# Performance work log

Measured on AMD Instinct MI355X. Metric: run time of the kernel, lower is better.

The kernel has to match this reference:

```python
import jax, jax.numpy as jnp
import numpy as np

D_HIDN = 64
SCALE = 1.0 / np.sqrt(D_HIDN).astype(np.float32)
MASK_FILL = -1e9


def setup_inputs() -> dict:
    key = jax.random.key(0)
    kq, kk, kv, km = jax.random.split(key, 4)
    B, H, S, D = 4, 16, 2048, 64
    Q = jax.random.normal(kq, (B, H, S, D), dtype=jnp.float32)
    K = jax.random.normal(kk, (B, H, S, D), dtype=jnp.float32)
    V = jax.random.normal(kv, (B, H, S, D), dtype=jnp.float32)
    attn_mask = jax.random.randint(km, (B, H, S, S), 0, 2).astype(jnp.bool_)
    return {"Q": Q, "K": K, "V": V, "attn_mask": attn_mask}


def reference(Q, K, V, attn_mask):
    # scores = Q K^T * scale  -> [B,H,S,S]
    scores = jnp.einsum("bhqd,bhkd->bhqk", Q, K) * SCALE
    scores = jnp.where(attn_mask, MASK_FILL, scores)
    attn_prob = jax.nn.softmax(scores, axis=-1)
    # dropout is identity in eval / deterministic reference
    context = jnp.einsum("bhqk,bhkd->bhqd", attn_prob, V)
    return (context, attn_prob)
```

## Files before the change

### kernel.cpp

```cpp
#include <hip/hip_runtime.h>
#include <stdint.h>

#define SEQ 2048
#define DIM 64
#define QBLK 16
#define NWAVE 8
#define KPW 256
#define NCT 16
#define NCHUNK 8
#define THREADS 512
#define SCALE 0.125f
#define LOG2E 1.4426950408889634f
#define PSTR 40
#define VPAD 18
#define NTSTR (32*VPAD + 8)

typedef __attribute__((ext_vector_type(4))) float f32x4;
typedef __attribute__((ext_vector_type(4))) int   i32x4;
typedef __attribute__((ext_vector_type(8))) __bf16 bf16x8;

static __device__ __forceinline__ unsigned bfbits(float x) {
    union { __bf16 b; unsigned short u; } cv; cv.b = (__bf16)x; return (unsigned)cv.u;
}
static __device__ __forceinline__ float lo16(unsigned u) { return __uint_as_float(u << 16); }
static __device__ __forceinline__ float hi16(unsigned u) { return __uint_as_float(u & 0xffff0000u); }
static __device__ __forceinline__ bf16x8 cvt8(f32x4 a, f32x4 b) {
    bf16x8 f;
    f[0]=(__bf16)a[0]; f[1]=(__bf16)a[1]; f[2]=(__bf16)a[2]; f[3]=(__bf16)a[3];
    f[4]=(__bf16)b[0]; f[5]=(__bf16)b[1]; f[6]=(__bf16)b[2]; f[7]=(__bf16)b[3];
    return f;
}

struct WaveBuf {
    union {
        __bf16 vbuf[4 * NTSTR];
        float  ctx[QBLK * DIM];
    };
};
struct SharedT {
    WaveBuf sw[NWAVE];
    __bf16 plds[NWAVE][QBLK][PSTR];
    float red_m[QBLK][NWAVE];
    float red_s[QBLK][NWAVE];
};

__global__ __launch_bounds__(THREADS, 4)
void sdpa_mfma11(const float* __restrict__ Q, const float* __restrict__ K,
                 const float* __restrict__ V, const int* __restrict__ mask,
                 float* __restrict__ ctx_out, float* __restrict__ prob_out) {
    __shared__ SharedT su;

    const int rb   = ((blockIdx.x & 7) << 10) + (blockIdx.x >> 3);
    const int bh   = rb >> 7;
    const int q0   = (rb & 127) * QBLK;
    const int t    = threadIdx.x;
    const int lane = t & 63;
    const int w    = t >> 6;
    const int g    = lane >> 4;
    const int c    = lane & 15;

    const size_t bh_off = (size_t)bh * SEQ * DIM;
    const float* Qb = Q + bh_off;
    const float* Kb = K + bh_off;
    const float* Vb = V + bh_off;
    const int*   Mb = mask + (size_t)bh * SEQ * SEQ;
    const int wbase = w * KPW;

    bf16x8 qf[2];
    {
        const float* qr = Qb + (size_t)(q0 + c) * DIM + 8 * g;
        qf[0] = cvt8(*(const f32x4*)(qr),      *(const f32x4*)(qr + 4));
        qf[1] = cvt8(*(const f32x4*)(qr + 32), *(const f32x4*)(qr + 36));
    }

    unsigned sc_pk[2 * NCT];
    f32x4 kr[4];
    i32x4 mraw[2];
    {
        const float* k0 = Kb + (size_t)(wbase + c) * DIM + 8 * g;
        kr[0] = *(const f32x4*)(k0);      kr[1] = *(const f32x4*)(k0 + 4);
        kr[2] = *(const f32x4*)(k0 + 32); kr[3] = *(const f32x4*)(k0 + 36);
        mraw[0] = *(const i32x4*)(Mb + (size_t)(q0 + c) * SEQ + wbase + 4 * g);
    }
    #pragma unroll
    for (int ct = 0; ct < NCT; ++ct) {
        if (ct + 1 < NCT)
            mraw[(ct + 1) & 1] = *(const i32x4*)(Mb + (size_t)(q0 + c) * SEQ + wbase + (ct + 1) * 16 + 4 * g);
        bf16x8 kf0 = cvt8(kr[0], kr[1]);
        bf16x8 kf1 = cvt8(kr[2], kr[3]);
        if (ct + 1 < NCT) {
            const float* kn = Kb + (size_t)(wbase + (ct + 1) * 16 + c) * DIM + 8 * g;
            kr[0] = *(const f32x4*)(kn);      kr[1] = *(const f32x4*)(kn + 4);
            kr[2] = *(const f32x4*)(kn + 32); kr[3] = *(const f32x4*)(kn + 36);
        }
        f32x4 acc = {0.f, 0.f, 0.f, 0.f};
        acc = __builtin_amdgcn_mfma_f32_16x16x32_bf16(kf0, qf[0], acc, 0, 0, 0);
        acc = __builtin_amdgcn_mfma_f32_16x16x32_bf16(kf1, qf[1], acc, 0, 0, 0);
        i32x4 mm = mraw[ct & 1];
        float x0 = mm[0] ? -1e9f : acc[0] * SCALE;
        float x1 = mm[1] ? -1e9f : acc[1] * SCALE;
        float x2 = mm[2] ? -1e9f : acc[2] * SCALE;
        float x3 = mm[3] ? -1e9f : acc[3] * SCALE;
        sc_pk[2 * ct]     = bfbits(x0) | (bfbits(x1) << 16);
        sc_pk[2 * ct + 1] = bfbits(x2) | (bfbits(x3) << 16);
    }

    float mx = -3e38f;
    #pragma unroll
    for (int i = 0; i < 2 * NCT; ++i)
        mx = fmaxf(mx, fmaxf(lo16(sc_pk[i]), hi16(sc_pk[i])));
    mx = fmaxf(mx, __shfl_xor(mx, 16));
    mx = fmaxf(mx, __shfl_xor(mx, 32));
    if (g == 0) su.red_m[c][w] = mx;
    __syncthreads();
    float M = su.red_m[c][0];
    #pragma unroll
    for (int i = 1; i < NWAVE; ++i) M = fmaxf(M, su.red_m[c][i]);

    float sum = 0.f;
    #pragma unroll
    for (int i = 0; i < 2 * NCT; ++i) {
        float e0 = exp2f((lo16(sc_pk[i]) - M) * LOG2E);
        float e1 = exp2f((hi16(sc_pk[i]) - M) * LOG2E);
        sum += e0 + e1;
        sc_pk[i] = bfbits(e0) | (bfbits(e1) << 16);
    }
    sum += __shfl_xor(sum, 16);
    sum += __shfl_xor(sum, 32);
    if (g == 0) su.red_s[c][w] = sum;
    __syncthreads();
    float S = 0.f;
    #pragma unroll
    for (int i = 0; i < NWAVE; ++i) S += su.red_s[c][i];
    const float inv = 1.0f / S;
    float invr[4];
    #pragma unroll
    for (int jr = 0; jr < 4; ++jr) invr[jr] = __shfl(inv, 4 * g + jr);

    f32x4 cacc[4];
    #pragma unroll
    for (int nt = 0; nt < 4; ++nt) cacc[nt] = (f32x4){0.f, 0.f, 0.f, 0.f};

    const int r_st = lane >> 4;
    const int cw   = (4 * c) & 15;
    const int ntw  = c >> 2;
    float* prow = prob_out + ((size_t)bh * SEQ + (q0 + c)) * SEQ + wbase;
    __bf16* vbufW = su.sw[w].vbuf;

    #pragma unroll
    for (int cc = 0; cc < NCHUNK; ++cc) {
        const float* vsrc = Vb + (size_t)(wbase + cc * 32 + r_st) * DIM + 4 * c;
        f32x4 vraw[4];
        #pragma unroll
        for (int i = 0; i < 4; ++i)
            vraw[i] = *(const f32x4*)(vsrc + (size_t)(4 * i) * DIM);
        #pragma unroll
        for (int i = 0; i < 4; ++i) {
            ushort2 lo_, hi_;
            lo_.x = (unsigned short)bfbits(vraw[i][0]);
            lo_.y = (unsigned short)bfbits(vraw[i][1]);
            hi_.x = (unsigned short)bfbits(vraw[i][2]);
            hi_.y = (unsigned short)bfbits(vraw[i][3]);
            __bf16* p = &vbufW[ntw * NTSTR + (4 * i + r_st) * VPAD + cw];
            *(ushort2*)p = lo_;
            *(ushort2*)(p + 2) = hi_;
        }
        #pragma unroll
        for (int i = 0; i < 4; ++i)
            vraw[i] = *(const f32x4*)(vsrc + (size_t)(16 + 4 * i) * DIM);
        #pragma unroll
        for (int i = 0; i < 4; ++i) {
            ushort2 lo_, hi_;
            lo_.x = (unsigned short)bfbits(vraw[i][0]);
            lo_.y = (unsigned short)bfbits(vraw[i][1]);
            hi_.x = (unsigned short)bfbits(vraw[i][2]);
            hi_.y = (unsigned short)bfbits(vraw[i][3]);
            __bf16* p = &vbufW[ntw * NTSTR + (16 + 4 * i + r_st) * VPAD + cw];
            *(ushort2*)p = lo_;
            *(ushort2*)(p + 2) = hi_;
        }

        unsigned pkA0 = sc_pk[4 * cc],     pkA1 = sc_pk[4 * cc + 1];
        unsigned pkB0 = sc_pk[4 * cc + 2], pkB1 = sc_pk[4 * cc + 3];
        {
            f32x4 pnA = { lo16(pkA0) * inv, hi16(pkA0) * inv, lo16(pkA1) * inv, hi16(pkA1) * inv };
            f32x4 pnB = { lo16(pkB0) * inv, hi16(pkB0) * inv, lo16(pkB1) * inv, hi16(pkB1) * inv };
            *(f32x4*)(prow + 32 * cc + 4 * g)      = pnA;
            *(f32x4*)(prow + 32 * cc + 16 + 4 * g) = pnB;
        }
        {
            uint2 ua; ua.x = pkA0; ua.y = pkA1;
            uint2 ub; ub.x = pkB0; ub.y = pkB1;
            *(uint2*)&su.plds[w][c][4 * g]      = ua;
            *(uint2*)&su.plds[w][c][16 + 4 * g] = ub;
        }
        bf16x8 pf = *(const bf16x8*)&su.plds[w][c][8 * g];

        bf16x8 vfr[4];
        #pragma unroll
        for (int nt = 0; nt < 4; ++nt) {
            bf16x8 f;
            #pragma unroll
            for (int j = 0; j < 8; ++j)
                f[j] = vbufW[nt * NTSTR + (8 * g + j) * VPAD + c];
            vfr[nt] = f;
        }

        __builtin_amdgcn_s_setprio(1);
        #pragma unroll
        for (int nt = 0; nt < 4; ++nt)
            cacc[nt] = __builtin_amdgcn_mfma_f32_16x16x32_bf16(pf, vfr[nt], cacc[nt], 0, 0, 0);
        __builtin_amdgcn_s_setprio(0);
    }

    #pragma unroll
    for (int nt = 0; nt < 4; ++nt)
        #pragma unroll
        for (int jr = 0; jr < 4; ++jr)
            su.sw[w].ctx[(4 * g + jr) * DIM + nt * 16 + c] = cacc[nt][jr] * invr[jr];
    __syncthreads();
    {
        int e = t * 2;
        float2 a = make_float2(0.f, 0.f);
        #pragma unroll
        for (int i = 0; i < NWAVE; ++i) {
            float2 v = *(const float2*)&su.sw[i].ctx[e];
            a.x += v.x; a.y += v.y;
        }
        *(float2*)(ctx_out + ((size_t)bh * SEQ + q0) * DIM + e) = a;
    }
}

extern "C" void kernel_launch(void* const* d_in, const int* in_sizes, int n_in,
                              void* d_out, int out_size, void* d_ws, size_t ws_size,
                              hipStream_t stream) {
    const float* Q = (const float*)d_in[0];
    const float* K = (const float*)d_in[1];
    const float* V = (const float*)d_in[2];
    const int* mask = (const int*)d_in[3];
    float* ctx  = (float*)d_out;
    float* prob = (float*)d_out + (size_t)4 * 16 * SEQ * DIM;

    dim3 grid(64 * (SEQ / QBLK));
    dim3 block(THREADS);
    sdpa_mfma11<<<grid, block, 0, stream>>>(Q, K, V, mask, ctx, prob);
}
```

Baseline: 1.032 ms.

## Batch mask loads into bitmasks and prefetch V chunks one step ahead

Mask loads become deep batches of four 16-int vectors that are compressed into 32-bit bitmasks. This raises memory-level parallelism on the mask stream, which is the largest input. Masking moves to a separate pass over the packed bf16 scores after the QK MFMA loop. V for the first chunk is loaded before the softmax reductions, and each later chunk is prefetched during the current one to hide global latency. The cost is more live registers (mask quads and V prefetch buffers), which could lower occupancy or cause spills.

```diff
diff --git a/kernel.cpp b/kernel.cpp
--- a/kernel.cpp
+++ b/kernel.cpp
@@ -30,6 +30,9 @@
     f[4]=(__bf16)b[0]; f[5]=(__bf16)b[1]; f[6]=(__bf16)b[2]; f[7]=(__bf16)b[3];
     return f;
 }
+static __device__ __forceinline__ unsigned nib4(i32x4 mm) {
+    return (mm[0]?1u:0u) | (mm[1]?2u:0u) | (mm[2]?4u:0u) | (mm[3]?8u:0u);
+}
 
 struct WaveBuf {
     union {
@@ -45,7 +48,7 @@
 };
 
 __global__ __launch_bounds__(THREADS, 4)
-void sdpa_mfma11(const float* __restrict__ Q, const float* __restrict__ K,
+void sdpa_mfma12(const float* __restrict__ Q, const float* __restrict__ K,
                  const float* __restrict__ V, const int* __restrict__ mask,
                  float* __restrict__ ctx_out, float* __restrict__ prob_out) {
     __shared__ SharedT su;
@@ -74,18 +77,40 @@
     }
 
     unsigned sc_pk[2 * NCT];
+    unsigned mbits0 = 0u, mbits1 = 0u;
+    const int* mrow = Mb + (size_t)(q0 + c) * SEQ + wbase + 4 * g;
+    i32x4 mq0[4], mq1[4];
+    #pragma unroll
+    for (int j = 0; j < 4; ++j) mq0[j] = *(const i32x4*)(mrow + 16 * j);
+    #pragma unroll
+    for (int j = 0; j < 4; ++j) mq1[j] = *(const i32x4*)(mrow + 16 * (4 + j));
+
     f32x4 kr[4];
-    i32x4 mraw[2];
     {
         const float* k0 = Kb + (size_t)(wbase + c) * DIM + 8 * g;
         kr[0] = *(const f32x4*)(k0);      kr[1] = *(const f32x4*)(k0 + 4);
         kr[2] = *(const f32x4*)(k0 + 32); kr[3] = *(const f32x4*)(k0 + 36);
-        mraw[0] = *(const i32x4*)(Mb + (size_t)(q0 + c) * SEQ + wbase + 4 * g);
-    }
+    }
+
     #pragma unroll
     for (int ct = 0; ct < NCT; ++ct) {
-        if (ct + 1 < NCT)
-            mraw[(ct + 1) & 1] = *(const i32x4*)(Mb + (size_t)(q0 + c) * SEQ + wbase + (ct + 1) * 16 + 4 * g);
+        if (ct == 4) {
+            #pragma unroll
+            for (int j = 0; j < 4; ++j) mbits0 |= nib4(mq0[j]) << (4 * j);
+            #pragma unroll
+            for (int j = 0; j < 4; ++j) mq0[j] = *(const i32x4*)(mrow + 16 * (8 + j));
+        }
+        if (ct == 8) {
+            #pragma unroll
+            for (int j = 0; j < 4; ++j) mbits0 |= nib4(mq1[j]) << (4 * (4 + j));
+            #pragma unroll
+            for (int j = 0; j < 4; ++j) mq1[j] = *(const i32x4*)(mrow + 16 * (12 + j));
+        }
+        if (ct == 12) {
+            #pragma unroll
+            for (int j = 0; j < 4; ++j) mbits1 |= nib4(mq0[j]) << (4 * j);
+        }
+
         bf16x8 kf0 = cvt8(kr[0], kr[1]);
         bf16x8 kf1 = cvt8(kr[2], kr[3]);
         if (ct + 1 < NCT) {
@@ -96,11 +121,33 @@
         f32x4 acc = {0.f, 0.f, 0.f, 0.f};
         acc = __builtin_amdgcn_mfma_f32_16x16x32_bf16(kf0, qf[0], acc, 0, 0, 0);
         acc = __builtin_amdgcn_mfma_f32_16x16x32_bf16(kf1, qf[1], acc, 0, 0, 0);
-        i32x4 mm = mraw[ct & 1];
-        float x0 = mm[0] ? -1e9f : acc[0] * SCALE;
-        float x1 = mm[1] ? -1e9f : acc[1] * SCALE;
-        float x2 = mm[2] ? -1e9f : acc[2] * SCALE;
-        float x3 = mm[3] ? -1e9f : acc[3] * SCALE;
+        sc_pk[2 * ct]     = bfbits(acc[0] * SCALE) | (bfbits(acc[1] * SCALE) << 16);
+        sc_pk[2 * ct + 1] = bfbits(acc[2] * SCALE) | (bfbits(acc[3] * SCALE) << 16);
+    }
+
+    const int r_st = lane >> 4;
+    const int cw   = (4 * c) & 15;
+    const int ntw  = c >> 2;
+    f32x4 vrawA[4], vrawB[4];
+    {
+        const float* vsrc = Vb + (size_t)(wbase + r_st) * DIM + 4 * c;
+        #pragma unroll
+        for (int i = 0; i < 4; ++i) {
+            vrawA[i] = *(const f32x4*)(vsrc + (size_t)(4 * i) * DIM);
+            vrawB[i] = *(const f32x4*)(vsrc + (size_t)(16 + 4 * i) * DIM);
+        }
+    }
+
+    #pragma unroll
+    for (int j = 0; j < 4; ++j) mbits1 |= nib4(mq1[j]) << (4 * (4 + j));
+
+    #pragma unroll
+    for (int ct = 0; ct < NCT; ++ct) {
+        unsigned nib = ((ct < 8) ? (mbits0 >> (4 * ct)) : (mbits1 >> (4 * (ct - 8)))) & 0xFu;
+        float x0 = (nib & 1u) ? -1e9f : lo16(sc_pk[2 * ct]);
+        float x1 = (nib & 2u) ? -1e9f : hi16(sc_pk[2 * ct]);
+        float x2 = (nib & 4u) ? -1e9f : lo16(sc_pk[2 * ct + 1]);
+        float x3 = (nib & 8u) ? -1e9f : hi16(sc_pk[2 * ct + 1]);
         sc_pk[2 * ct]     = bfbits(x0) | (bfbits(x1) << 16);
         sc_pk[2 * ct + 1] = bfbits(x2) | (bfbits(x3) << 16);
     }
@@ -141,43 +188,40 @@
     #pragma unroll
     for (int nt = 0; nt < 4; ++nt) cacc[nt] = (f32x4){0.f, 0.f, 0.f, 0.f};
 
-    const int r_st = lane >> 4;
-    const int cw   = (4 * c) & 15;
-    const int ntw  = c >> 2;
     float* prow = prob_out + ((size_t)bh * SEQ + (q0 + c)) * SEQ + wbase;
     __bf16* vbufW = su.sw[w].vbuf;
 
     #pragma unroll
     for (int cc = 0; cc < NCHUNK; ++cc) {
-        const float* vsrc = Vb + (size_t)(wbase + cc * 32 + r_st) * DIM + 4 * c;
-        f32x4 vraw[4];
-        #pragma unroll
-        for (int i = 0; i < 4; ++i)
-            vraw[i] = *(const f32x4*)(vsrc + (size_t)(4 * i) * DIM);
         #pragma unroll
         for (int i = 0; i < 4; ++i) {
             ushort2 lo_, hi_;
-            lo_.x = (unsigned short)bfbits(vraw[i][0]);
-            lo_.y = (unsigned short)bfbits(vraw[i][1]);
-            hi_.x = (unsigned short)bfbits(vraw[i][2]);
-            hi_.y = (unsigned short)bfbits(vraw[i][3]);
+            lo_.x = (unsigned short)bfbits(vrawA[i][0]);
+            lo_.y = (unsigned short)bfbits(vrawA[i][1]);
+            hi_.x = (unsigned short)bfbits(vrawA[i][2]);
+            hi_.y = (unsigned short)bfbits(vrawA[i][3]);
             __bf16* p = &vbufW[ntw * NTSTR + (4 * i + r_st) * VPAD + cw];
             *(ushort2*)p = lo_;
             *(ushort2*)(p + 2) = hi_;
         }
         #pragma unroll
-        for (int i = 0; i < 4; ++i)
-            vraw[i] = *(const f32x4*)(vsrc + (size_t)(16 + 4 * i) * DIM);
-        #pragma unroll
         for (int i = 0; i < 4; ++i) {
             ushort2 lo_, hi_;
-            lo_.x = (unsigned short)bfbits(vraw[i][0]);
-            lo_.y = (unsigned short)bfbits(vraw[i][1]);
-            hi_.x = (unsigned short)bfbits(vraw[i][2]);
-            hi_.y = (unsigned short)bfbits(vraw[i][3]);
+            lo_.x = (unsigned short)bfbits(vrawB[i][0]);
+            lo_.y = (unsigned short)bfbits(vrawB[i][1]);
+            hi_.x = (unsigned short)bfbits(vrawB[i][2]);
+            hi_.y = (unsigned short)bfbits(vrawB[i][3]);
             __bf16* p = &vbufW[ntw * NTSTR + (16 + 4 * i + r_st) * VPAD + cw];
             *(ushort2*)p = lo_;
             *(ushort2*)(p + 2) = hi_;
+        }
+        if (cc + 1 < NCHUNK) {
+            const float* vsrc = Vb + (size_t)(wbase + (cc + 1) * 32 + r_st) * DIM + 4 * c;
+            #pragma unroll
+            for (int i = 0; i < 4; ++i) {
+                vrawA[i] = *(const f32x4*)(vsrc + (size_t)(4 * i) * DIM);
+                vrawB[i] = *(const f32x4*)(vsrc + (size_t)(16 + 4 * i) * DIM);
+            }
         }
 
         unsigned pkA0 = sc_pk[4 * cc],     pkA1 = sc_pk[4 * cc + 1];
@@ -243,5 +287,5 @@
 
     dim3 grid(64 * (SEQ / QBLK));
     dim3 block(THREADS);
-    sdpa_mfma11<<<grid, block, 0, stream>>>(Q, K, V, mask, ctx, prob);
-}
+    sdpa_mfma12<<<grid, block, 0, stream>>>(Q, K, V, mask, ctx, prob);
+}
```

Result: faster. 1.010 ms (-2.1%).

## Process two 16-row query blocks per workgroup with wave-local softmax stats

Applied to the files above, without the earlier changes.

Each workgroup now handles 32 query rows as two 16-row halves, so the bf16 V tiles staged in LDS feed MFMAs for both halves. This halves the V reloads and conversions per query row and halves the grid. Softmax max and sum are computed per wave and merged across waves with exp rescaling, which drops one block barrier. The mask is batch-loaded and packed into bit nibbles to overlap its global reads with the QK^T MFMAs, and the V loads are software-pipelined. In exchange, register pressure rises from holding two score arrays, and occupancy may drop under the launch bound of four blocks.

```diff
diff --git a/kernel.cpp b/kernel.cpp
--- a/kernel.cpp
+++ b/kernel.cpp
@@ -6,7 +6,6 @@
 #define QBLK 16
 #define NWAVE 8
 #define KPW 256
-#define NCT 16
 #define NCHUNK 8
 #define THREADS 512
 #define SCALE 0.125f
@@ -29,6 +28,9 @@
     f[0]=(__bf16)a[0]; f[1]=(__bf16)a[1]; f[2]=(__bf16)a[2]; f[3]=(__bf16)a[3];
     f[4]=(__bf16)b[0]; f[5]=(__bf16)b[1]; f[6]=(__bf16)b[2]; f[7]=(__bf16)b[3];
     return f;
+}
+static __device__ __forceinline__ unsigned nib4(i32x4 mm) {
+    return (mm[0]?1u:0u) | (mm[1]?2u:0u) | (mm[2]?4u:0u) | (mm[3]?8u:0u);
 }
 
 struct WaveBuf {
@@ -39,20 +41,82 @@
 };
 struct SharedT {
     WaveBuf sw[NWAVE];
-    __bf16 plds[NWAVE][QBLK][PSTR];
-    float red_m[QBLK][NWAVE];
-    float red_s[QBLK][NWAVE];
+    __bf16 pldsA[NWAVE][QBLK][PSTR];
+    __bf16 pldsB[NWAVE][QBLK][PSTR];
+    float red_m[2][QBLK][NWAVE];
+    float red_s[2][QBLK][NWAVE];
 };
 
+#define QKT_HALF(MROWP, QFP, SCP, MBITSV, TB, LASTH)                           \
+  {                                                                            \
+    i32x4 mq0_ = *(const i32x4*)((MROWP) + 16*((TB)+0));                       \
+    i32x4 mq1_ = *(const i32x4*)((MROWP) + 16*((TB)+1));                       \
+    i32x4 mq2_ = *(const i32x4*)((MROWP) + 16*((TB)+2));                       \
+    i32x4 mq3_ = *(const i32x4*)((MROWP) + 16*((TB)+3));                       \
+    i32x4 mq4_ = *(const i32x4*)((MROWP) + 16*((TB)+4));                       \
+    i32x4 mq5_ = *(const i32x4*)((MROWP) + 16*((TB)+5));                       \
+    i32x4 mq6_ = *(const i32x4*)((MROWP) + 16*((TB)+6));                       \
+    i32x4 mq7_ = *(const i32x4*)((MROWP) + 16*((TB)+7));                       \
+    __builtin_amdgcn_sched_barrier(0);                                         \
+    _Pragma("unroll")                                                          \
+    for (int ct_ = 0; ct_ < 8; ++ct_) {                                        \
+      if (ct_ == 3)                                                            \
+        MBITSV |= nib4(mq0_) | (nib4(mq1_) << 4) | (nib4(mq2_) << 8)           \
+                  | (nib4(mq3_) << 12);                                        \
+      bf16x8 kf0_ = cvt8(kr[0], kr[1]);                                        \
+      bf16x8 kf1_ = cvt8(kr[2], kr[3]);                                        \
+      if (!(LASTH) || ct_ < 7) {                                               \
+        const int nti_ = ((TB) + ct_ + 1) & 15;                                \
+        const float* kn_ = Kb + (size_t)(wbase + nti_ * 16 + c) * DIM + 8 * g; \
+        kr[0] = *(const f32x4*)(kn_);      kr[1] = *(const f32x4*)(kn_ + 4);   \
+        kr[2] = *(const f32x4*)(kn_ + 32); kr[3] = *(const f32x4*)(kn_ + 36);  \
+      }                                                                        \
+      f32x4 acc_ = {0.f, 0.f, 0.f, 0.f};                                       \
+      acc_ = __builtin_amdgcn_mfma_f32_16x16x32_bf16(kf0_, (QFP)[0], acc_, 0, 0, 0); \
+      acc_ = __builtin_amdgcn_mfma_f32_16x16x32_bf16(kf1_, (QFP)[1], acc_, 0, 0, 0); \
+      (SCP)[2*((TB)+ct_)]   = bfbits(acc_[0]*SCALE) | (bfbits(acc_[1]*SCALE) << 16); \
+      (SCP)[2*((TB)+ct_)+1] = bfbits(acc_[2]*SCALE) | (bfbits(acc_[3]*SCALE) << 16); \
+    }                                                                          \
+    MBITSV |= (nib4(mq4_) << 16) | (nib4(mq5_) << 20) | (nib4(mq6_) << 24)     \
+              | (nib4(mq7_) << 28);                                            \
+  }
+
+#define SMAX_SWEEP(SCP, MB0, MB1, MXV, SSV)                                    \
+  float MXV = -3e38f;                                                          \
+  _Pragma("unroll")                                                            \
+  for (int ct_ = 0; ct_ < 16; ++ct_) {                                         \
+    unsigned nib_ = ((ct_ < 8) ? ((MB0) >> (4*ct_)) : ((MB1) >> (4*(ct_-8)))) & 0xFu; \
+    float x0_ = (nib_ & 1u) ? -1e9f : lo16((SCP)[2*ct_]);                      \
+    float x1_ = (nib_ & 2u) ? -1e9f : hi16((SCP)[2*ct_]);                      \
+    float x2_ = (nib_ & 4u) ? -1e9f : lo16((SCP)[2*ct_+1]);                    \
+    float x3_ = (nib_ & 8u) ? -1e9f : hi16((SCP)[2*ct_+1]);                    \
+    (SCP)[2*ct_]   = bfbits(x0_) | (bfbits(x1_) << 16);                        \
+    (SCP)[2*ct_+1] = bfbits(x2_) | (bfbits(x3_) << 16);                        \
+    MXV = fmaxf(MXV, fmaxf(fmaxf(x0_, x1_), fmaxf(x2_, x3_)));                 \
+  }                                                                            \
+  MXV = fmaxf(MXV, __shfl_xor(MXV, 16));                                       \
+  MXV = fmaxf(MXV, __shfl_xor(MXV, 32));                                       \
+  float SSV = 0.f;                                                             \
+  _Pragma("unroll")                                                            \
+  for (int i_ = 0; i_ < 32; ++i_) {                                            \
+    float e0_ = exp2f((lo16((SCP)[i_]) - MXV) * LOG2E);                        \
+    float e1_ = exp2f((hi16((SCP)[i_]) - MXV) * LOG2E);                        \
+    SSV += e0_ + e1_;                                                          \
+    (SCP)[i_] = bfbits(e0_) | (bfbits(e1_) << 16);                             \
+  }                                                                            \
+  SSV += __shfl_xor(SSV, 16);                                                  \
+  SSV += __shfl_xor(SSV, 32);
+
 __global__ __launch_bounds__(THREADS, 4)
-void sdpa_mfma11(const float* __restrict__ Q, const float* __restrict__ K,
+void sdpa_mfma14(const float* __restrict__ Q, const float* __restrict__ K,
                  const float* __restrict__ V, const int* __restrict__ mask,
                  float* __restrict__ ctx_out, float* __restrict__ prob_out) {
     __shared__ SharedT su;
 
-    const int rb   = ((blockIdx.x & 7) << 10) + (blockIdx.x >> 3);
-    const int bh   = rb >> 7;
-    const int q0   = (rb & 127) * QBLK;
+    const int bid  = blockIdx.x;
+    const int rb   = ((bid & 7) << 9) | (bid >> 3);
+    const int bh   = rb >> 6;
+    const int q0   = (rb & 63) * 32;
     const int t    = threadIdx.x;
     const int lane = t & 63;
     const int w    = t >> 6;
@@ -66,94 +130,105 @@
     const int*   Mb = mask + (size_t)bh * SEQ * SEQ;
     const int wbase = w * KPW;
 
-    bf16x8 qf[2];
+    const int* mrowA = Mb + (size_t)(q0 + c) * SEQ + wbase + 4 * g;
+    const int* mrowB = Mb + (size_t)(q0 + 16 + c) * SEQ + wbase + 4 * g;
+
+    bf16x8 qfA[2];
     {
         const float* qr = Qb + (size_t)(q0 + c) * DIM + 8 * g;
-        qf[0] = cvt8(*(const f32x4*)(qr),      *(const f32x4*)(qr + 4));
-        qf[1] = cvt8(*(const f32x4*)(qr + 32), *(const f32x4*)(qr + 36));
-    }
-
-    unsigned sc_pk[2 * NCT];
+        qfA[0] = cvt8(*(const f32x4*)(qr),      *(const f32x4*)(qr + 4));
+        qfA[1] = cvt8(*(const f32x4*)(qr + 32), *(const f32x4*)(qr + 36));
+    }
     f32x4 kr[4];
-    i32x4 mraw[2];
     {
         const float* k0 = Kb + (size_t)(wbase + c) * DIM + 8 * g;
         kr[0] = *(const f32x4*)(k0);      kr[1] = *(const f32x4*)(k0 + 4);
         kr[2] = *(const f32x4*)(k0 + 32); kr[3] = *(const f32x4*)(k0 + 36);
-        mraw[0] = *(const i32x4*)(Mb + (size_t)(q0 + c) * SEQ + wbase + 4 * g);
-    }
-    #pragma unroll
-    for (int ct = 0; ct < NCT; ++ct) {
-        if (ct + 1 < NCT)
-            mraw[(ct + 1) & 1] = *(const i32x4*)(Mb + (size_t)(q0 + c) * SEQ + wbase + (ct + 1) * 16 + 4 * g);
-        bf16x8 kf0 = cvt8(kr[0], kr[1]);
-        bf16x8 kf1 = cvt8(kr[2], kr[3]);
-        if (ct + 1 < NCT) {
-            const float* kn = Kb + (size_t)(wbase + (ct + 1) * 16 + c) * DIM + 8 * g;
-            kr[0] = *(const f32x4*)(kn);      kr[1] = *(const f32x4*)(kn + 4);
-            kr[2] = *(const f32x4*)(kn + 32); kr[3] = *(const f32x4*)(kn + 36);
-        }
-        f32x4 acc = {0.f, 0.f, 0.f, 0.f};
-        acc = __builtin_amdgcn_mfma_f32_16x16x32_bf16(kf0, qf[0], acc, 0, 0, 0);
-        acc = __builtin_amdgcn_mfma_f32_16x16x32_bf16(kf1, qf[1], acc, 0, 0, 0);
-        i32x4 mm = mraw[ct & 1];
-        float x0 = mm[0] ? -1e9f : acc[0] * SCALE;
-        float x1 = mm[1] ? -1e9f : acc[1] * SCALE;
-        float x2 = mm[2] ? -1e9f : acc[2] * SCALE;
-        float x3 = mm[3] ? -1e9f : acc[3] * SCALE;
-        sc_pk[2 * ct]     = bfbits(x0) | (bfbits(x1) << 16);
-        sc_pk[2 * ct + 1] = bfbits(x2) | (bfbits(x3) << 16);
-    }
-
-    float mx = -3e38f;
-    #pragma unroll
-    for (int i = 0; i < 2 * NCT; ++i)
-        mx = fmaxf(mx, fmaxf(lo16(sc_pk[i]), hi16(sc_pk[i])));
-    mx = fmaxf(mx, __shfl_xor(mx, 16));
-    mx = fmaxf(mx, __shfl_xor(mx, 32));
-    if (g == 0) su.red_m[c][w] = mx;
-    __syncthreads();
-    float M = su.red_m[c][0];
-    #pragma unroll
-    for (int i = 1; i < NWAVE; ++i) M = fmaxf(M, su.red_m[c][i]);
-
-    float sum = 0.f;
-    #pragma unroll
-    for (int i = 0; i < 2 * NCT; ++i) {
-        float e0 = exp2f((lo16(sc_pk[i]) - M) * LOG2E);
-        float e1 = exp2f((hi16(sc_pk[i]) - M) * LOG2E);
-        sum += e0 + e1;
-        sc_pk[i] = bfbits(e0) | (bfbits(e1) << 16);
-    }
-    sum += __shfl_xor(sum, 16);
-    sum += __shfl_xor(sum, 32);
-    if (g == 0) su.red_s[c][w] = sum;
-    __syncthreads();
-    float S = 0.f;
-    #pragma unroll
-    for (int i = 0; i < NWAVE; ++i) S += su.red_s[c][i];
-    const float inv = 1.0f / S;
-    float invr[4];
-    #pragma unroll
-    for (int jr = 0; jr < 4; ++jr) invr[jr] = __shfl(inv, 4 * g + jr);
-
-    f32x4 cacc[4];
-    #pragma unroll
-    for (int nt = 0; nt < 4; ++nt) cacc[nt] = (f32x4){0.f, 0.f, 0.f, 0.f};
+    }
+
+    unsigned sc_pkA[32], sc_pkB[32];
+    unsigned mbA0 = 0u, mbA1 = 0u, mbB0 = 0u, mbB1 = 0u;
+
+    QKT_HALF(mrowA, qfA, sc_pkA, mbA0, 0, 0)
+    QKT_HALF(mrowA, qfA, sc_pkA, mbA1, 8, 0)
+    SMAX_SWEEP(sc_pkA, mbA0, mbA1, mxA, ssA)
+
+    bf16x8 qfB[2];
+    {
+        const float* qr = Qb + (size_t)(q0 + 16 + c) * DIM + 8 * g;
+        qfB[0] = cvt8(*(const f32x4*)(qr),      *(const f32x4*)(qr + 4));
+        qfB[1] = cvt8(*(const f32x4*)(qr + 32), *(const f32x4*)(qr + 36));
+    }
+    QKT_HALF(mrowB, qfB, sc_pkB, mbB0, 0, 0)
+    QKT_HALF(mrowB, qfB, sc_pkB, mbB1, 8, 1)
+    SMAX_SWEEP(sc_pkB, mbB0, mbB1, mxB, ssB)
+
+    if (g == 0) {
+        su.red_m[0][c][w] = mxA; su.red_s[0][c][w] = ssA;
+        su.red_m[1][c][w] = mxB; su.red_s[1][c][w] = ssB;
+    }
 
     const int r_st = lane >> 4;
     const int cw   = (4 * c) & 15;
     const int ntw  = c >> 2;
-    float* prow = prob_out + ((size_t)bh * SEQ + (q0 + c)) * SEQ + wbase;
-    __bf16* vbufW = su.sw[w].vbuf;
-
-    #pragma unroll
-    for (int cc = 0; cc < NCHUNK; ++cc) {
-        const float* vsrc = Vb + (size_t)(wbase + cc * 32 + r_st) * DIM + 4 * c;
-        f32x4 vraw[4];
+    f32x4 vraw[4];
+    {
+        const float* vsrc = Vb + (size_t)(wbase + r_st) * DIM + 4 * c;
         #pragma unroll
         for (int i = 0; i < 4; ++i)
             vraw[i] = *(const f32x4*)(vsrc + (size_t)(4 * i) * DIM);
+    }
+
+    __syncthreads();
+
+    float facA, facB;
+    {
+        float M = su.red_m[0][c][0];
+        #pragma unroll
+        for (int i = 1; i < NWAVE; ++i) M = fmaxf(M, su.red_m[0][c][i]);
+        float S = 0.f;
+        #pragma unroll
+        for (int i = 0; i < NWAVE; ++i)
+            S += su.red_s[0][c][i] * exp2f((su.red_m[0][c][i] - M) * LOG2E);
+        facA = exp2f((mxA - M) * LOG2E) / S;
+    }
+    {
+        float M = su.red_m[1][c][0];
+        #pragma unroll
+        for (int i = 1; i < NWAVE; ++i) M = fmaxf(M, su.red_m[1][c][i]);
+        float S = 0.f;
+        #pragma unroll
+        for (int i = 0; i < NWAVE; ++i)
+            S += su.red_s[1][c][i] * exp2f((su.red_m[1][c][i] - M) * LOG2E);
+        facB = exp2f((mxB - M) * LOG2E) / S;
+    }
+
+    f32x4 caccA[4], caccB[4];
+    #pragma unroll
+    for (int nt = 0; nt < 4; ++nt) {
+        caccA[nt] = (f32x4){0.f, 0.f, 0.f, 0.f};
+        caccB[nt] = (f32x4){0.f, 0.f, 0.f, 0.f};
+    }
+    float* prowA = prob_out + ((size_t)bh * SEQ + q0 + c) * SEQ + wbase;
+    float* prowB = prowA + (size_t)16 * SEQ;
+    __bf16* vbufW = su.sw[w].vbuf;
+
+    #pragma unroll
+    for (int cc = 0; cc < NCHUNK; ++cc) {
+        bf16x8 pfA;
+        {
+            unsigned a0 = sc_pkA[4*cc], a1 = sc_pkA[4*cc+1];
+            unsigned a2 = sc_pkA[4*cc+2], a3 = sc_pkA[4*cc+3];
+            f32x4 pn0 = { lo16(a0)*facA, hi16(a0)*facA, lo16(a1)*facA, hi16(a1)*facA };
+            f32x4 pn1 = { lo16(a2)*facA, hi16(a2)*facA, lo16(a3)*facA, hi16(a3)*facA };
+            *(f32x4*)(prowA + 32*cc + 4*g)      = pn0;
+            *(f32x4*)(prowA + 32*cc + 16 + 4*g) = pn1;
+            uint2 ua; ua.x = a0; ua.y = a1;
+            uint2 ub; ub.x = a2; ub.y = a3;
+            *(uint2*)&su.pldsA[w][c][4*g]      = ua;
+            *(uint2*)&su.pldsA[w][c][16+4*g]   = ub;
+            pfA = *(const bf16x8*)&su.pldsA[w][c][8*g];
+        }
         #pragma unroll
         for (int i = 0; i < 4; ++i) {
             ushort2 lo_, hi_;
@@ -161,13 +236,30 @@
             lo_.y = (unsigned short)bfbits(vraw[i][1]);
             hi_.x = (unsigned short)bfbits(vraw[i][2]);
             hi_.y = (unsigned short)bfbits(vraw[i][3]);
-            __bf16* p = &vbufW[ntw * NTSTR + (4 * i + r_st) * VPAD + cw];
+            __bf16* p = &vbufW[ntw * NTSTR + (4*i + r_st) * VPAD + cw];
             *(ushort2*)p = lo_;
             *(ushort2*)(p + 2) = hi_;
         }
-        #pragma unroll
-        for (int i = 0; i < 4; ++i)
-            vraw[i] = *(const f32x4*)(vsrc + (size_t)(16 + 4 * i) * DIM);
+        {
+            const float* vsrc = Vb + (size_t)(wbase + cc*32 + 16 + r_st) * DIM + 4*c;
+            #pragma unroll
+            for (int i = 0; i < 4; ++i)
+                vraw[i] = *(const f32x4*)(vsrc + (size_t)(4 * i) * DIM);
+        }
+        bf16x8 pfB;
+        {
+            unsigned b0 = sc_pkB[4*cc], b1 = sc_pkB[4*cc+1];
+            unsigned b2 = sc_pkB[4*cc+2], b3 = sc_pkB[4*cc+3];
+            f32x4 pn0 = { lo16(b0)*facB, hi16(b0)*facB, lo16(b1)*facB, hi16(b1)*facB };
+            f32x4 pn1 = { lo16(b2)*facB, hi16(b2)*facB, lo16(b3)*facB, hi16(b3)*facB };
+            *(f32x4*)(prowB + 32*cc + 4*g)      = pn0;
+            *(f32x4*)(prowB + 32*cc + 16 + 4*g) = pn1;
+            uint2 ua; ua.x = b0; ua.y = b1;
+            uint2 ub; ub.x = b2; ub.y = b3;
+            *(uint2*)&su.pldsB[w][c][4*g]      = ua;
+            *(uint2*)&su.pldsB[w][c][16+4*g]   = ub;
+            pfB = *(const bf16x8*)&su.pldsB[w][c][8*g];
+        }
         #pragma unroll
         for (int i = 0; i < 4; ++i) {
             ushort2 lo_, hi_;
@@ -175,49 +267,45 @@
             lo_.y = (unsigned short)bfbits(vraw[i][1]);
             hi_.x = (unsigned short)bfbits(vraw[i][2]);
             hi_.y = (unsigned short)bfbits(vraw[i][3]);
-            __bf16* p = &vbufW[ntw * NTSTR + (16 + 4 * i + r_st) * VPAD + cw];
+            __bf16* p = &vbufW[ntw * NTSTR + (16 + 4*i + r_st) * VPAD + cw];
             *(ushort2*)p = lo_;
             *(ushort2*)(p + 2) = hi_;
         }
-
-        unsigned pkA0 = sc_pk[4 * cc],     pkA1 = sc_pk[4 * cc + 1];
-        unsigned pkB0 = sc_pk[4 * cc + 2], pkB1 = sc_pk[4 * cc + 3];
-        {
-            f32x4 pnA = { lo16(pkA0) * inv, hi16(pkA0) * inv, lo16(pkA1) * inv, hi16(pkA1) * inv };
-            f32x4 pnB = { lo16(pkB0) * inv, hi16(pkB0) * inv, lo16(pkB1) * inv, hi16(pkB1) * inv };
-            *(f32x4*)(prow + 32 * cc + 4 * g)      = pnA;
-            *(f32x4*)(prow + 32 * cc + 16 + 4 * g) = pnB;
-        }
-        {
-            uint2 ua; ua.x = pkA0; ua.y = pkA1;
-            uint2 ub; ub.x = pkB0; ub.y = pkB1;
-            *(uint2*)&su.plds[w][c][4 * g]      = ua;
-            *(uint2*)&su.plds[w][c][16 + 4 * g] = ub;
-        }
-        bf16x8 pf = *(const bf16x8*)&su.plds[w][c][8 * g];
-
+        if (cc + 1 < NCHUNK) {
+            const float* vsrc = Vb + (size_t)(wbase + (cc+1)*32 + r_st) * DIM + 4*c;
+            #pragma unroll
+            for (int i = 0; i < 4; ++i)
+                vraw[i] = *(const f32x4*)(vsrc + (size_t)(4 * i) * DIM);
+        }
         bf16x8 vfr[4];
         #pragma unroll
         for (int nt = 0; nt < 4; ++nt) {
             bf16x8 f;
             #pragma unroll
             for (int j = 0; j < 8; ++j)
-                f[j] = vbufW[nt * NTSTR + (8 * g + j) * VPAD + c];
+                f[j] = vbufW[nt * NTSTR + (8*g + j) * VPAD + c];
             vfr[nt] = f;
         }
-
         __builtin_amdgcn_s_setprio(1);
         #pragma unroll
-        for (int nt = 0; nt < 4; ++nt)
-            cacc[nt] = __builtin_amdgcn_mfma_f32_16x16x32_bf16(pf, vfr[nt], cacc[nt], 0, 0, 0);
+        for (int nt = 0; nt < 4; ++nt) {
+            caccA[nt] = __builtin_amdgcn_mfma_f32_16x16x32_bf16(pfA, vfr[nt], caccA[nt], 0, 0, 0);
+            caccB[nt] = __builtin_amdgcn_mfma_f32_16x16x32_bf16(pfB, vfr[nt], caccB[nt], 0, 0, 0);
+        }
         __builtin_amdgcn_s_setprio(0);
     }
 
+    float invrA[4], invrB[4];
+    #pragma unroll
+    for (int jr = 0; jr < 4; ++jr) {
+        invrA[jr] = __shfl(facA, 4*g + jr);
+        invrB[jr] = __shfl(facB, 4*g + jr);
+    }
     #pragma unroll
     for (int nt = 0; nt < 4; ++nt)
         #pragma unroll
         for (int jr = 0; jr < 4; ++jr)
-            su.sw[w].ctx[(4 * g + jr) * DIM + nt * 16 + c] = cacc[nt][jr] * invr[jr];
+            su.sw[w].ctx[(4*g + jr) * DIM + nt*16 + c] = caccA[nt][jr] * invrA[jr];
     __syncthreads();
     {
         int e = t * 2;
@@ -228,6 +316,23 @@
             a.x += v.x; a.y += v.y;
         }
         *(float2*)(ctx_out + ((size_t)bh * SEQ + q0) * DIM + e) = a;
+    }
+    __syncthreads();
+    #pragma unroll
+    for (int nt = 0; nt < 4; ++nt)
+        #pragma unroll
+        for (int jr = 0; jr < 4; ++jr)
+            su.sw[w].ctx[(4*g + jr) * DIM + nt*16 + c] = caccB[nt][jr] * invrB[jr];
+    __syncthreads();
+    {
+        int e = t * 2;
+        float2 a = make_float2(0.f, 0.f);
+        #pragma unroll
+        for (int i = 0; i < NWAVE; ++i) {
+            float2 v = *(const float2*)&su.sw[i].ctx[e];
+            a.x += v.x; a.y += v.y;
+        }
+        *(float2*)(ctx_out + ((size_t)bh * SEQ + q0 + 16) * DIM + e) = a;
     }
 }
 
@@ -241,7 +346,7 @@
     float* ctx  = (float*)d_out;
     float* prob = (float*)d_out + (size_t)4 * 16 * SEQ * DIM;
 
-    dim3 grid(64 * (SEQ / QBLK));
+    dim3 grid(64 * (SEQ / 32));
     dim3 block(THREADS);
-    sdpa_mfma11<<<grid, block, 0, stream>>>(Q, K, V, mask, ctx, prob);
-}
+    sdpa_mfma14<<<grid, block, 0, stream>>>(Q, K, V, mask, ctx, prob);
+}
```

Result: slower. 1.738 ms (+68.4%).
